# Kernel optimization log

Hardware: AMD Instinct MI355X
Metric: run time of the kernel (lower is better)

Reference implementation:

```python
import jax, jax.numpy as jnp
import numpy as np

N, K, IN_C, OUT_C = 100000, 128, 128, 128


def setup_inputs() -> dict:
    key = jax.random.key(0)
    k1, k2, k3 = jax.random.split(key, 3)
    x = jax.random.normal(k1, (N, IN_C), dtype=jnp.float32)
    U = jax.random.normal(k2, (N, K), dtype=jnp.float32)
    coeffs = jax.random.normal(k3, (OUT_C, K, IN_C), dtype=jnp.float32)
    return {"x": x, "U": U, "coeffs": coeffs}


def reference(x, U, coeffs):
    # U.T @ x : (K, in_channels)
    spec = jnp.einsum('nk,ni->ki', U, x)
    # coeffs * spec, summed over in_channels : (out_channels, K)
    mixed = jnp.einsum('oki,ki->ok', coeffs, spec)
    # U @ mixed : (out_channels, N)
    out = jnp.einsum('nk,ok->on', U, mixed)
    # softmax over N (dim=-1), then transpose -> (N, out_channels)
    return jax.nn.softmax(out, axis=-1).T
```

## Files before the change

kernel.cpp:

```cpp
#include <hip/hip_runtime.h>
#include <math.h>

#define N_PTS 100000
#define KDIM 128
#define CDIM 128
#define TILE_N 64
#define NB1 ((N_PTS + TILE_N - 1) / TILE_N)

typedef short s16x8 __attribute__((ext_vector_type(8)));
typedef float f32x4 __attribute__((ext_vector_type(4)));

static __device__ __forceinline__ unsigned short f2bf(float f) {
    unsigned int u = __float_as_uint(f);
    unsigned int r = (u + 0x7FFFu + ((u >> 16) & 1u)) >> 16;
    return (unsigned short)r;
}
static __device__ __forceinline__ float bf2f(unsigned short h) {
    return __uint_as_float(((unsigned int)h) << 16);
}

__global__ __launch_bounds__(256) void kA(const float* __restrict__ U,
                                          const float* __restrict__ x,
                                          float* __restrict__ partials,
                                          int chunk) {
    __shared__ float Us[32 * 128];
    __shared__ float Xs[32 * 128];
    const int tid = threadIdx.x;
    const int b = blockIdx.x;
    const int n_begin = b * chunk;
    const int n_end = min(N_PTS, n_begin + chunk);
    const int tk = tid >> 4;
    const int ti = tid & 15;
    float acc[8][8];
#pragma unroll
    for (int a = 0; a < 8; ++a)
#pragma unroll
        for (int c = 0; c < 8; ++c) acc[a][c] = 0.0f;

    for (int n0 = n_begin; n0 < n_end; n0 += 32) {
#pragma unroll
        for (int r = 0; r < 4; ++r) {
            int idx = (r * 256 + tid) * 4;
            int n = idx >> 7;
            int k = idx & 127;
            int gn = n0 + n;
            float4 u4 = make_float4(0, 0, 0, 0), x4 = make_float4(0, 0, 0, 0);
            if (gn < n_end) {
                u4 = *(const float4*)&U[(size_t)gn * 128 + k];
                x4 = *(const float4*)&x[(size_t)gn * 128 + k];
            }
            *(float4*)&Us[n * 128 + k] = u4;
            *(float4*)&Xs[n * 128 + k] = x4;
        }
        __syncthreads();
        int nn = min(32, n_end - n0);
        for (int n = 0; n < nn; ++n) {
            float4 ua = *(float4*)&Us[n * 128 + tk * 8];
            float4 ub = *(float4*)&Us[n * 128 + tk * 8 + 4];
            float4 xa = *(float4*)&Xs[n * 128 + ti * 8];
            float4 xb = *(float4*)&Xs[n * 128 + ti * 8 + 4];
            float u[8] = {ua.x, ua.y, ua.z, ua.w, ub.x, ub.y, ub.z, ub.w};
            float xv[8] = {xa.x, xa.y, xa.z, xa.w, xb.x, xb.y, xb.z, xb.w};
#pragma unroll
            for (int a = 0; a < 8; ++a)
#pragma unroll
                for (int c = 0; c < 8; ++c) acc[a][c] += u[a] * xv[c];
        }
        __syncthreads();
    }
    float* p = partials + (size_t)b * 16384;
#pragma unroll
    for (int a = 0; a < 8; ++a)
#pragma unroll
        for (int c = 0; c < 8; c += 4) {
            *(float4*)&p[(tk * 8 + a) * 128 + ti * 8 + c] =
                make_float4(acc[a][c], acc[a][c + 1], acc[a][c + 2], acc[a][c + 3]);
        }
}

__global__ __launch_bounds__(256) void kA2a(const float* __restrict__ partials,
                                            float* __restrict__ partial2, int nA) {
    const int jc = blockIdx.x >> 3;
    const int s = blockIdx.x & 7;
    const int j = jc * 256 + threadIdx.x;
    const int per = (nA + 7) >> 3;
    int b = s * per;
    const int be = min(b + per, nA);
    float a0 = 0.0f, a1 = 0.0f, a2 = 0.0f, a3 = 0.0f;
    for (; b + 4 <= be; b += 4) {
        a0 += partials[(size_t)(b + 0) * 16384 + j];
        a1 += partials[(size_t)(b + 1) * 16384 + j];
        a2 += partials[(size_t)(b + 2) * 16384 + j];
        a3 += partials[(size_t)(b + 3) * 16384 + j];
    }
    for (; b < be; ++b) a0 += partials[(size_t)b * 16384 + j];
    partial2[(size_t)s * 16384 + j] = (a0 + a1) + (a2 + a3);
}

__global__ __launch_bounds__(256) void kA2b(const float* __restrict__ partial2,
                                            float* __restrict__ spec) {
    int j = blockIdx.x * 256 + threadIdx.x;
    float v0 = partial2[j];
    float v1 = partial2[16384 + j];
    float v2 = partial2[2 * 16384 + j];
    float v3 = partial2[3 * 16384 + j];
    float v4 = partial2[4 * 16384 + j];
    float v5 = partial2[5 * 16384 + j];
    float v6 = partial2[6 * 16384 + j];
    float v7 = partial2[7 * 16384 + j];
    spec[j] = ((v0 + v1) + (v2 + v3)) + ((v4 + v5) + (v6 + v7));
}

__global__ __launch_bounds__(256) void kB(const float* __restrict__ coeffs,
                                          const float* __restrict__ spec,
                                          unsigned short* __restrict__ afrag_hi,
                                          unsigned short* __restrict__ afrag_lo) {
    int wave = (blockIdx.x * 256 + threadIdx.x) >> 6;
    int lane = threadIdx.x & 63;
    int o = wave >> 7;
    int k = wave & 127;
    float2 c2 = *(const float2*)&coeffs[((size_t)o * 128 + k) * 128 + lane * 2];
    float2 s2 = *(const float2*)&spec[k * 128 + lane * 2];
    float v = c2.x * s2.x + c2.y * s2.y;
#pragma unroll
    for (int s = 32; s >= 1; s >>= 1) v += __shfl_xor(v, s);
    if (lane == 0) {
        unsigned short hi = f2bf(v);
        unsigned short lo = f2bf(v - bf2f(hi));
        int idx = ((o >> 4) * 4 + (k >> 5)) * 512 + (((k >> 3) & 3) * 16 + (o & 15)) * 8 + (k & 7);
        afrag_hi[idx] = hi;
        afrag_lo[idx] = lo;
    }
}

__global__ __launch_bounds__(512) void kC1(const float* __restrict__ U,
                                           const unsigned short* __restrict__ afrag_hi,
                                           const unsigned short* __restrict__ afrag_lo,
                                           float* __restrict__ out,
                                           float* __restrict__ m_part,
                                           float* __restrict__ l_part) {
    __shared__ unsigned short Bh[8192];
    __shared__ unsigned short Bl[8192];
    const int tid = threadIdx.x;
    const int b = blockIdx.x;
    const int n0 = b * TILE_N;
    const int lane = tid & 63;
    const int w = tid >> 6;
    const int quad = lane >> 4;
    const int nl = lane & 15;

#pragma unroll
    for (int r = 0; r < 4; ++r) {
        int idx = (r * 512 + tid) * 4;
        int n = idx >> 7;
        int k = idx & 127;
        int gn = n0 + n;
        float4 u4 = (gn < N_PTS) ? *(const float4*)&U[(size_t)gn * 128 + k]
                                 : make_float4(0, 0, 0, 0);
        unsigned short h0 = f2bf(u4.x), h1 = f2bf(u4.y), h2 = f2bf(u4.z), h3 = f2bf(u4.w);
        unsigned short l0 = f2bf(u4.x - bf2f(h0));
        unsigned short l1 = f2bf(u4.y - bf2f(h1));
        unsigned short l2 = f2bf(u4.z - bf2f(h2));
        unsigned short l3 = f2bf(u4.w - bf2f(h3));
        int dst = ((k >> 5) * 4 + (n >> 4)) * 512 + (((k >> 3) & 3) * 16 + (n & 15)) * 8 + (k & 7);
        uint2 hp, lp;
        hp.x = (unsigned int)h0 | ((unsigned int)h1 << 16);
        hp.y = (unsigned int)h2 | ((unsigned int)h3 << 16);
        lp.x = (unsigned int)l0 | ((unsigned int)l1 << 16);
        lp.y = (unsigned int)l2 | ((unsigned int)l3 << 16);
        *(uint2*)&Bh[dst] = hp;
        *(uint2*)&Bl[dst] = lp;
    }

    s16x8 Ah[4], Al[4];
#pragma unroll
    for (int kc = 0; kc < 4; ++kc) {
        size_t aoff = (size_t)(w * 4 + kc) * 512 + lane * 8;
        Ah[kc] = *(const s16x8*)(afrag_hi + aoff);
        Al[kc] = *(const s16x8*)(afrag_lo + aoff);
    }

    __syncthreads();

    f32x4 acc[4];
#pragma unroll
    for (int nt = 0; nt < 4; ++nt) acc[nt] = (f32x4)(0.0f);

#pragma unroll
    for (int kc = 0; kc < 4; ++kc) {
#pragma unroll
        for (int nt = 0; nt < 4; ++nt) {
            int boff = ((kc * 4 + nt) * 512) + lane * 8;
            s16x8 bh = *(s16x8*)&Bh[boff];
            s16x8 bl = *(s16x8*)&Bl[boff];
            acc[nt] = __builtin_amdgcn_mfma_f32_16x16x32_bf16(Ah[kc], bh, acc[nt], 0, 0, 0);
            acc[nt] = __builtin_amdgcn_mfma_f32_16x16x32_bf16(Al[kc], bh, acc[nt], 0, 0, 0);
            acc[nt] = __builtin_amdgcn_mfma_f32_16x16x32_bf16(Ah[kc], bl, acc[nt], 0, 0, 0);
        }
    }

#pragma unroll
    for (int nt = 0; nt < 4; ++nt) {
        if (n0 + nt * 16 + nl >= N_PTS) {
#pragma unroll
            for (int reg = 0; reg < 4; ++reg) acc[nt][reg] = -3.4e38f;
        }
    }

    float mb[4];
#pragma unroll
    for (int reg = 0; reg < 4; ++reg)
        mb[reg] = fmaxf(fmaxf(acc[0][reg], acc[1][reg]), fmaxf(acc[2][reg], acc[3][reg]));
#pragma unroll
    for (int s = 1; s < 16; s <<= 1) {
#pragma unroll
        for (int reg = 0; reg < 4; ++reg) mb[reg] = fmaxf(mb[reg], __shfl_xor(mb[reg], s));
    }

#pragma unroll
    for (int nt = 0; nt < 4; ++nt) {
#pragma unroll
        for (int reg = 0; reg < 4; ++reg) acc[nt][reg] = __expf(acc[nt][reg] - mb[reg]);
        int gn = n0 + nt * 16 + nl;
        if (gn < N_PTS)
            *(f32x4*)&out[(size_t)gn * 128 + w * 16 + quad * 4] = acc[nt];
    }

    float ls[4];
#pragma unroll
    for (int reg = 0; reg < 4; ++reg)
        ls[reg] = ((acc[0][reg] + acc[1][reg]) + (acc[2][reg] + acc[3][reg]));
#pragma unroll
    for (int s = 1; s < 16; s <<= 1) {
#pragma unroll
        for (int reg = 0; reg < 4; ++reg) ls[reg] += __shfl_xor(ls[reg], s);
    }

    if (nl == 0) {
#pragma unroll
        for (int reg = 0; reg < 4; ++reg) {
            int o = w * 16 + quad * 4 + reg;
            m_part[(size_t)o * NB1 + b] = mb[reg];
            l_part[(size_t)o * NB1 + b] = ls[reg];
        }
    }
}

__global__ __launch_bounds__(256) void kC2(const float* __restrict__ m_part,
                                           const float* __restrict__ l_part,
                                           float* __restrict__ scale) {
    const int o = blockIdx.x;
    const int tid = threadIdx.x;
    const float* __restrict__ mp = m_part + (size_t)o * NB1;
    const float* __restrict__ lp = l_part + (size_t)o * NB1;
    __shared__ float sm[256];
    float m = -3.4e38f;
    for (int b = tid; b < NB1; b += 256) m = fmaxf(m, mp[b]);
    sm[tid] = m;
    __syncthreads();
    for (int s = 128; s >= 1; s >>= 1) {
        if (tid < s) sm[tid] = fmaxf(sm[tid], sm[tid + s]);
        __syncthreads();
    }
    m = sm[0];
    __syncthreads();
    float l = 0.0f;
    for (int b = tid; b < NB1; b += 256)
        l += lp[b] * __expf(mp[b] - m);
    sm[tid] = l;
    __syncthreads();
    for (int s = 128; s >= 1; s >>= 1) {
        if (tid < s) sm[tid] += sm[tid + s];
        __syncthreads();
    }
    l = sm[0];
    float inv = 1.0f / l;
    for (int b = tid; b < NB1; b += 256)
        scale[(size_t)o * NB1 + b] = __expf(mp[b] - m) * inv;
}

__global__ __launch_bounds__(256) void kC3(float* __restrict__ out,
                                           const float* __restrict__ scale) {
    const int b = blockIdx.x;
    const int tid = threadIdx.x;
    __shared__ float sc[128];
    if (tid < 128) sc[tid] = scale[(size_t)tid * NB1 + b];
    __syncthreads();
    const int n0 = b * TILE_N;
#pragma unroll
    for (int r = 0; r < 8; ++r) {
        int idx = (r * 256 + tid) * 4;
        int n = idx >> 7;
        int o = idx & 127;
        int gn = n0 + n;
        if (gn < N_PTS) {
            float4 v = *(float4*)&out[(size_t)gn * 128 + o];
            v.x *= sc[o];
            v.y *= sc[o + 1];
            v.z *= sc[o + 2];
            v.w *= sc[o + 3];
            *(float4*)&out[(size_t)gn * 128 + o] = v;
        }
    }
}

extern "C" void kernel_launch(void* const* d_in, const int* in_sizes, int n_in,
                              void* d_out, int out_size, void* d_ws, size_t ws_size,
                              hipStream_t stream) {
    const float* x = (const float*)d_in[0];
    const float* U = (const float*)d_in[1];
    const float* coeffs = (const float*)d_in[2];
    float* out = (float*)d_out;

    float* f = (float*)d_ws;
    float* spec = f;
    unsigned short* afrag_hi = (unsigned short*)(f + 16384);
    unsigned short* afrag_lo = (unsigned short*)(f + 16384 + 8192);
    float* m_part = f + 16384 + 16384;
    float* l_part = m_part + (size_t)128 * NB1;
    float* scale = l_part + (size_t)128 * NB1;
    float* partial2 = scale + (size_t)128 * NB1;
    float* partialsA = partial2 + 8 * 16384;

    size_t fixed_bytes = ((size_t)(16384 * 2) + (size_t)NB1 * 128 * 3 + (size_t)8 * 16384) * 4;
    int nA = 512;
    if (ws_size > fixed_bytes) {
        size_t avail = (ws_size - fixed_bytes) / 65536;
        if ((size_t)nA > avail) nA = (int)avail;
    } else {
        nA = 1;
    }
    if (nA < 1) nA = 1;
    int chunk = (N_PTS + nA - 1) / nA;

    kA<<<nA, 256, 0, stream>>>(U, x, partialsA, chunk);
    kA2a<<<512, 256, 0, stream>>>(partialsA, partial2, nA);
    kA2b<<<64, 256, 0, stream>>>(partial2, spec);
    kB<<<4096, 256, 0, stream>>>(coeffs, spec, afrag_hi, afrag_lo);
    kC1<<<NB1, 512, 0, stream>>>(U, afrag_hi, afrag_lo, out, m_part, l_part);
    kC2<<<128, 256, 0, stream>>>(m_part, l_part, scale);
    kC3<<<NB1, 256, 0, stream>>>(out, scale);
}
```

Before: 230.8 us.

## Compute U^T x with split-bf16 MFMA instead of fp32 FMA

Rewrites the first reduction kernel (U^T @ x) to run on MFMA 16x16x32 bf16 instructions. Each fp32 value is split into high and low bf16 parts, and three MFMAs per tile (hi*hi, lo*hi, hi*lo) approximate fp32 accuracy. Operands are staged in LDS in a fragment-friendly layout. The aim is to replace the scalar FMA outer-product loop with matrix-core throughput. The costs are extra split arithmetic, scalar rather than vectorized global loads, uncoalesced scalar partial stores, and a small accuracy loss from dropping the lo*lo term.

Measured after the change: 206.8 us. -10.4%, faster.

```diff
diff --git a/kernel.cpp b/kernel.cpp
--- a/kernel.cpp
+++ b/kernel.cpp
@@ -19,63 +19,106 @@
     return __uint_as_float(((unsigned int)h) << 16);
 }
 
+static __device__ __forceinline__ void split_trunc(float v, unsigned short& hi, unsigned short& lo) {
+    unsigned int u = __float_as_uint(v);
+    unsigned int uh = u & 0xFFFF0000u;
+    float lf = v - __uint_as_float(uh);
+    hi = (unsigned short)(u >> 16);
+    lo = (unsigned short)(__float_as_uint(lf) >> 16);
+}
+
+static __device__ __forceinline__ int frag_dst(int nloc, int c) {
+    return (c >> 4) * 512 + (((nloc >> 3) & 3) * 16 + (c & 15)) * 8 + (nloc & 7);
+}
+
 __global__ __launch_bounds__(256) void kA(const float* __restrict__ U,
                                           const float* __restrict__ x,
                                           float* __restrict__ partials,
                                           int chunk) {
-    __shared__ float Us[32 * 128];
-    __shared__ float Xs[32 * 128];
+    __shared__ unsigned short Ah_[4096], Al_[4096], Bh_[4096], Bl_[4096];
     const int tid = threadIdx.x;
     const int b = blockIdx.x;
     const int n_begin = b * chunk;
     const int n_end = min(N_PTS, n_begin + chunk);
-    const int tk = tid >> 4;
-    const int ti = tid & 15;
-    float acc[8][8];
-#pragma unroll
-    for (int a = 0; a < 8; ++a)
-#pragma unroll
-        for (int c = 0; c < 8; ++c) acc[a][c] = 0.0f;
+    const int lane = tid & 63;
+    const int w = tid >> 6;
+    const int mtb = (w >> 1) * 4;
+    const int ntb = (w & 1) * 4;
+    const int quad = lane >> 4;
+    const int nl = lane & 15;
+
+    const int sc = tid & 127;
+    const int sqh = tid >> 7;
+
+    f32x4 acc[4][4];
+#pragma unroll
+    for (int mi = 0; mi < 4; ++mi)
+#pragma unroll
+        for (int ni = 0; ni < 4; ++ni) acc[mi][ni] = (f32x4)(0.0f);
 
     for (int n0 = n_begin; n0 < n_end; n0 += 32) {
 #pragma unroll
-        for (int r = 0; r < 4; ++r) {
-            int idx = (r * 256 + tid) * 4;
-            int n = idx >> 7;
-            int k = idx & 127;
-            int gn = n0 + n;
-            float4 u4 = make_float4(0, 0, 0, 0), x4 = make_float4(0, 0, 0, 0);
-            if (gn < n_end) {
-                u4 = *(const float4*)&U[(size_t)gn * 128 + k];
-                x4 = *(const float4*)&x[(size_t)gn * 128 + k];
+        for (int p = 0; p < 2; ++p) {
+            const int q = sqh * 2 + p;
+            const int nb = q * 8;
+            float uv[8], xv[8];
+#pragma unroll
+            for (int jj = 0; jj < 8; ++jj) {
+                int gn = n0 + nb + jj;
+                bool ok = (gn < n_end);
+                uv[jj] = ok ? U[(size_t)gn * 128 + sc] : 0.0f;
+                xv[jj] = ok ? x[(size_t)gn * 128 + sc] : 0.0f;
             }
-            *(float4*)&Us[n * 128 + k] = u4;
-            *(float4*)&Xs[n * 128 + k] = x4;
+            s16x8 uh, ul, xh, xl;
+#pragma unroll
+            for (int jj = 0; jj < 8; ++jj) {
+                unsigned short h, l;
+                split_trunc(uv[jj], h, l);
+                uh[jj] = (short)h; ul[jj] = (short)l;
+                split_trunc(xv[jj], h, l);
+                xh[jj] = (short)h; xl[jj] = (short)l;
+            }
+            int dst = frag_dst(nb, sc);
+            *(s16x8*)&Ah_[dst] = uh;
+            *(s16x8*)&Al_[dst] = ul;
+            *(s16x8*)&Bh_[dst] = xh;
+            *(s16x8*)&Bl_[dst] = xl;
         }
         __syncthreads();
-        int nn = min(32, n_end - n0);
-        for (int n = 0; n < nn; ++n) {
-            float4 ua = *(float4*)&Us[n * 128 + tk * 8];
-            float4 ub = *(float4*)&Us[n * 128 + tk * 8 + 4];
-            float4 xa = *(float4*)&Xs[n * 128 + ti * 8];
-            float4 xb = *(float4*)&Xs[n * 128 + ti * 8 + 4];
-            float u[8] = {ua.x, ua.y, ua.z, ua.w, ub.x, ub.y, ub.z, ub.w};
-            float xv[8] = {xa.x, xa.y, xa.z, xa.w, xb.x, xb.y, xb.z, xb.w};
-#pragma unroll
-            for (int a = 0; a < 8; ++a)
-#pragma unroll
-                for (int c = 0; c < 8; ++c) acc[a][c] += u[a] * xv[c];
+
+        s16x8 ah[4], al[4];
+#pragma unroll
+        for (int mi = 0; mi < 4; ++mi) {
+            ah[mi] = *(s16x8*)&Ah_[(mtb + mi) * 512 + lane * 8];
+            al[mi] = *(s16x8*)&Al_[(mtb + mi) * 512 + lane * 8];
+        }
+#pragma unroll
+        for (int ni = 0; ni < 4; ++ni) {
+            s16x8 bh = *(s16x8*)&Bh_[(ntb + ni) * 512 + lane * 8];
+            s16x8 bl = *(s16x8*)&Bl_[(ntb + ni) * 512 + lane * 8];
+#pragma unroll
+            for (int mi = 0; mi < 4; ++mi) {
+                acc[mi][ni] = __builtin_amdgcn_mfma_f32_16x16x32_bf16(ah[mi], bh, acc[mi][ni], 0, 0, 0);
+                acc[mi][ni] = __builtin_amdgcn_mfma_f32_16x16x32_bf16(al[mi], bh, acc[mi][ni], 0, 0, 0);
+                acc[mi][ni] = __builtin_amdgcn_mfma_f32_16x16x32_bf16(ah[mi], bl, acc[mi][ni], 0, 0, 0);
+            }
         }
         __syncthreads();
     }
+
     float* p = partials + (size_t)b * 16384;
 #pragma unroll
-    for (int a = 0; a < 8; ++a)
-#pragma unroll
-        for (int c = 0; c < 8; c += 4) {
-            *(float4*)&p[(tk * 8 + a) * 128 + ti * 8 + c] =
-                make_float4(acc[a][c], acc[a][c + 1], acc[a][c + 2], acc[a][c + 3]);
-        }
+    for (int mi = 0; mi < 4; ++mi) {
+#pragma unroll
+        for (int reg = 0; reg < 4; ++reg) {
+            int k = (mtb + mi) * 16 + quad * 4 + reg;
+#pragma unroll
+            for (int ni = 0; ni < 4; ++ni) {
+                int i = (ntb + ni) * 16 + nl;
+                p[k * 128 + i] = acc[mi][ni][reg];
+            }
+        }
+    }
 }
 
 __global__ __launch_bounds__(256) void kA2a(const float* __restrict__ partials,
```
